# Kernel tuning notes

Hardware: AMD Instinct MI355X
Metric: run time of the kernel (lower is better)

Reference implementation:

```python
import jax, jax.numpy as jnp
import numpy as np

B, T, D, H = 4, 2048, 1024, 32  # batch, positions, embed_dim, max_history (buffer full)
DECAY_RATE = 0.95


def setup_inputs() -> dict:
    key = jax.random.key(0)
    ks = jax.random.split(key, 10)
    s = 1.0 / np.sqrt(D)
    return {
        "x": jax.random.normal(ks[0], (B, T, D), dtype=jnp.float32),
        "history": jax.random.normal(ks[1], (T, H, D), dtype=jnp.float32),
        "Wq": jax.random.normal(ks[2], (D, D), dtype=jnp.float32) * s,
        "bq": jax.random.normal(ks[3], (D,), dtype=jnp.float32) * 0.01,
        "Wk": jax.random.normal(ks[4], (D, D), dtype=jnp.float32) * s,
        "bk": jax.random.normal(ks[5], (D,), dtype=jnp.float32) * 0.01,
        "Wv": jax.random.normal(ks[6], (D, D), dtype=jnp.float32) * s,
        "bv": jax.random.normal(ks[7], (D,), dtype=jnp.float32) * 0.01,
        "Wo": jax.random.normal(ks[8], (D, D), dtype=jnp.float32) * s,
        "bo": jax.random.normal(ks[9], (D,), dtype=jnp.float32) * 0.01,
        "decay": jnp.power(jnp.float32(DECAY_RATE), jnp.arange(H, dtype=jnp.float32)),
    }


def reference(x, history, Wq, bq, Wk, bk, Wv, bv, Wo, bo, decay):
    # x: [B,T,D]; history: [T,H,D] (each position's own time history)
    d = x.shape[-1]
    Q = x @ Wq.T + bq                    # [B,T,D]
    K = history @ Wk.T + bk              # [T,H,D]
    V = history @ Wv.T + bv              # [T,H,D]
    # per-position attention over own history slice
    scores = jnp.einsum('btd,thd->bth', Q, K) / jnp.sqrt(jnp.float32(d))  # [B,T,H]
    bias = jnp.log(decay[::-1] + 1e-10)  # flipped log-decay, [H]
    attn = jax.nn.softmax(scores + bias, axis=-1)
    attended = jnp.einsum('bth,thd->btd', attn, V)  # [B,T,D]
    return (attended + x) @ Wo.T + bo
```

## Files before the change

kernel.cpp:

```cpp
#include <hip/hip_runtime.h>
#include <stdint.h>

#define B_ 4
#define T_ 2048
#define D_ 1024
#define H_ 32

typedef unsigned short u16;
typedef __attribute__((ext_vector_type(8))) short bf16x8;
typedef __attribute__((ext_vector_type(4))) float f32x4;

__device__ __forceinline__ u16 f2bf(float f) {
  union { float f; unsigned u; } c; c.f = f;
  unsigned r = 0x7fffu + ((c.u >> 16) & 1u);
  return (u16)((c.u + r) >> 16);
}
__device__ __forceinline__ float bf2f(u16 h) {
  union { unsigned u; float f; } c; c.u = ((unsigned)h) << 16;
  return c.f;
}

__device__ __forceinline__ void gload_lds16(const void* g, void* l) {
  __builtin_amdgcn_global_load_lds(
      (const __attribute__((address_space(1))) void*)g,
      (__attribute__((address_space(3))) void*)l, 16, 0, 0);
}

__global__ void megaprep(const float* __restrict__ x,
                         const float* __restrict__ Wq, const float* __restrict__ Wk,
                         const float* __restrict__ Wv, const float* __restrict__ Wo,
                         const float* __restrict__ bq, const float* __restrict__ bv,
                         const float* __restrict__ bo,
                         u16* __restrict__ xb,
                         u16* __restrict__ wqtb, u16* __restrict__ wktb,
                         u16* __restrict__ wvtb, u16* __restrict__ wob,
                         u16* __restrict__ b2w,
                         float* __restrict__ b2part, float* __restrict__ bvo) {
  const int bid = blockIdx.x;
  const int tid = threadIdx.x;
  if (bid < 4096) {
    const int z = bid >> 10, tile = bid & 1023;
    const int tx = tid & 31, ty = tid >> 5;
    const int c0 = (tile & 31) * 32, r0 = (tile >> 5) * 32;
    if (z == 3) {
#pragma unroll
      for (int r = 0; r < 32; r += 8) {
        const int row = r0 + ty + r, col = c0 + tx;
        const u16 v = f2bf(Wo[(size_t)row * D_ + col]);
        wob[(size_t)row * D_ + col] = v;
        b2w[(size_t)(D_ + row) * D_ + col] = v;
      }
      return;
    }
    const float* in = (z == 0) ? Wq : (z == 1) ? Wk : Wv;
    u16* out = (z == 0) ? wqtb : (z == 1) ? wktb : wvtb;
    __shared__ float tile_s[32][33];
#pragma unroll
    for (int r = 0; r < 32; r += 8)
      tile_s[ty + r][tx] = in[(size_t)(r0 + ty + r) * D_ + c0 + tx];
    __syncthreads();
#pragma unroll
    for (int r = 0; r < 32; r += 8)
      out[(size_t)(c0 + ty + r) * D_ + r0 + tx] = f2bf(tile_s[tx][ty + r]);
  } else if (bid < 6144) {
    const int base = (bid - 4096) * 1024;
#pragma unroll
    for (int k = 0; k < 4; ++k) {
      const int i4 = base + k * 256 + tid;
      float4 v = reinterpret_cast<const float4*>(x)[i4];
      ushort4 o;
      o.x = f2bf(v.x); o.y = f2bf(v.y); o.z = f2bf(v.z); o.w = f2bf(v.w);
      *reinterpret_cast<ushort4*>(xb + (size_t)i4 * 4) = o;
    }
  } else if (bid < 6208) {
    const int sub = bid - 6144;
    const int col = (sub & 3) * 256 + tid;
    const int j0 = (sub >> 2) * 64;
    float acc = 0.f;
#pragma unroll 8
    for (int j = 0; j < 64; ++j) acc += bq[j0 + j] * Wk[(size_t)(j0 + j) * D_ + col];
    b2part[(sub >> 2) * D_ + col] = acc;
  } else {
    const int wid = tid >> 6, lane = tid & 63;
    const int j = (bid - 6208) * 4 + wid;
    float acc = 0.f;
#pragma unroll
    for (int k4 = lane; k4 < 256; k4 += 64) {
      float4 w = *reinterpret_cast<const float4*>(Wo + (size_t)j * D_ + k4 * 4);
      float4 b = *reinterpret_cast<const float4*>(bv + k4 * 4);
      acc += w.x * b.x + w.y * b.y + w.z * b.z + w.w * b.w;
    }
#pragma unroll
    for (int m = 1; m < 64; m <<= 1) acc += __shfl_xor(acc, m);
    if (lane == 0) bvo[j] = acc + bo[j];
  }
}

__global__ void finish_kernel(const float* __restrict__ pk, const float* __restrict__ b2part,
                              const float* __restrict__ decay,
                              u16* __restrict__ b2w, u16* __restrict__ wvo,
                              float* __restrict__ bias2, float* __restrict__ logb) {
  const int bid = blockIdx.x;
  const int tid = threadIdx.x;
  if (bid < 2048) {
    const int tgt = bid >> 10;
    const int i4 = (bid & 1023) * 256 + tid;
    const int row = i4 >> 8, c4 = i4 & 255;
    const size_t slab = (size_t)D_ * D_;
    const size_t base = (size_t)tgt * 4 * slab + (size_t)row * D_ + c4 * 4;
    float4 a = *reinterpret_cast<const float4*>(pk + base);
    float4 b = *reinterpret_cast<const float4*>(pk + slab + base);
    float4 c = *reinterpret_cast<const float4*>(pk + 2 * slab + base);
    float4 d = *reinterpret_cast<const float4*>(pk + 3 * slab + base);
    ushort4 o;
    o.x = f2bf(a.x + b.x + c.x + d.x);
    o.y = f2bf(a.y + b.y + c.y + d.y);
    o.z = f2bf(a.z + b.z + c.z + d.z);
    o.w = f2bf(a.w + b.w + c.w + d.w);
    u16* out = tgt ? wvo : b2w;
    *reinterpret_cast<ushort4*>(out + (size_t)row * D_ + c4 * 4) = o;
  } else {
    const int col = (bid - 2048) * 256 + tid;
    float acc = 0.f;
#pragma unroll
    for (int jb = 0; jb < 16; ++jb) acc += b2part[jb * D_ + col];
    bias2[col] = acc;
    bias2[D_ + col] = 0.f;
    if (bid == 2048 && tid < H_)
      logb[tid] = __logf(decay[H_ - 1 - tid] + 1e-10f);
  }
}

template<int OUT_BF16, int ADDX>
__device__ __forceinline__ void gemm_core(
    const u16* __restrict__ A, const u16* __restrict__ Bw,
    const float* __restrict__ bias, const u16* __restrict__ xadd, int ldx,
    void* __restrict__ Cv, int K, int lda, int ldb, int ldc, int bm, int bn) {
  __shared__ u16 lA[128 * 32];
  __shared__ u16 lB[128 * 32];
  const int tid = threadIdx.x;
  const int w = tid >> 6, lane = tid & 63;
  const int wr = w >> 1, wc = w & 1;
  const int lr = lane & 15;
  const int lk = (lane >> 4) << 3;

  f32x4 acc[4][4] = {};

  const int c0 = tid, c1 = tid + 256;
  const size_t aoff0 = (size_t)(bm * 128 + (c0 >> 2)) * lda + ((c0 & 3) << 3);
  const size_t aoff1 = (size_t)(bm * 128 + (c1 >> 2)) * lda + ((c1 & 3) << 3);
  const size_t boff0 = (size_t)(bn * 128 + (c0 >> 2)) * ldb + ((c0 & 3) << 3);
  const size_t boff1 = (size_t)(bn * 128 + (c1 >> 2)) * ldb + ((c1 & 3) << 3);
  u16* lA0 = lA + c0 * 8; u16* lA1 = lA + c1 * 8;
  u16* lB0 = lB + c0 * 8; u16* lB1 = lB + c1 * 8;

  for (int k0 = 0; k0 < K; k0 += 32) {
    gload_lds16(A + aoff0 + k0, lA0);
    gload_lds16(A + aoff1 + k0, lA1);
    gload_lds16(Bw + boff0 + k0, lB0);
    gload_lds16(Bw + boff1 + k0, lB1);
    __syncthreads();
    bf16x8 aF[4], bF[4];
#pragma unroll
    for (int m = 0; m < 4; ++m)
      aF[m] = *reinterpret_cast<const bf16x8*>(&lA[(wr * 64 + m * 16 + lr) * 32 + lk]);
#pragma unroll
    for (int n = 0; n < 4; ++n)
      bF[n] = *reinterpret_cast<const bf16x8*>(&lB[(wc * 64 + n * 16 + lr) * 32 + lk]);
#pragma unroll
    for (int m = 0; m < 4; ++m)
#pragma unroll
      for (int n = 0; n < 4; ++n)
        acc[m][n] = __builtin_amdgcn_mfma_f32_16x16x32_bf16(aF[m], bF[n], acc[m][n], 0, 0, 0);
    __syncthreads();
  }

#pragma unroll
  for (int m = 0; m < 4; ++m) {
    const int row = bm * 128 + wr * 64 + m * 16 + ((lane >> 4) << 2);
#pragma unroll
    for (int n = 0; n < 4; ++n) {
      const int col = bn * 128 + wc * 64 + n * 16 + lr;
      const float bb = bias ? bias[col] : 0.f;
#pragma unroll
      for (int r = 0; r < 4; ++r) {
        float v = acc[m][n][r] + bb;
        if (ADDX) v += bf2f(xadd[(size_t)(row + r) * ldx + col]);
        if (OUT_BF16) ((u16*)Cv)[(size_t)(row + r) * ldc + col] = f2bf(v);
        else          ((float*)Cv)[(size_t)(row + r) * ldc + col] = v;
      }
    }
  }
}

template<int OUT_BF16, int ADDX>
__global__ __launch_bounds__(256, 2)
void gemm_bt(const u16* __restrict__ A, const u16* __restrict__ Bw,
             const float* __restrict__ bias, const u16* __restrict__ xadd, int ldx,
             void* __restrict__ Cv, int K, int lda, int ldb, int ldc) {
  gemm_core<OUT_BF16, ADDX>(A, Bw, bias, xadd, ldx, Cv, K, lda, ldb, ldc,
                            blockIdx.x, blockIdx.y);
}

__global__ __launch_bounds__(256, 2)
void gemm_splitk_dual(const u16* __restrict__ wktb, const u16* __restrict__ wqtb,
                      const u16* __restrict__ wob, const u16* __restrict__ wvtb,
                      float* __restrict__ pk) {
  const int z = blockIdx.z;
  const u16 *A, *B;
  if (z < 4) { A = wktb + z * 256; B = wqtb + z * 256; }
  else       { A = wob + (z - 4) * 256; B = wvtb + (z - 4) * 256; }
  float* C = pk + (size_t)z * D_ * D_;
  gemm_core<0, 0>(A, B, nullptr, nullptr, 0, C, 256, D_, D_, D_,
                  blockIdx.x, blockIdx.y);
}

__global__ __launch_bounds__(256, 2)
void attn_kernel(const u16* __restrict__ Q2, const float* __restrict__ hist,
                 const float* __restrict__ logb, u16* __restrict__ hw) {
  __shared__ u16 lh[H_ * D_];
  __shared__ float sTab[4][H_];
  __shared__ float pTab[H_][4];
  const int t = blockIdx.x;
  const int tid = threadIdx.x;
  const int w = tid >> 6, lane = tid & 63;
  const float* hp = hist + (size_t)t * (H_ * D_);

  float s[32] = {};
#pragma unroll 2
  for (int c = 0; c < 4; ++c) {
    const int d0 = lane * 4 + 256 * c;
    float qf[4][4];
#pragma unroll
    for (int b = 0; b < 4; ++b) {
      ushort4 qv = *reinterpret_cast<const ushort4*>(Q2 + ((size_t)b * T_ + t) * 2048 + d0);
      qf[b][0] = bf2f(qv.x); qf[b][1] = bf2f(qv.y);
      qf[b][2] = bf2f(qv.z); qf[b][3] = bf2f(qv.w);
    }
#pragma unroll
    for (int i = 0; i < 8; ++i) {
      const int h = w * 8 + i;
      float4 hv = *reinterpret_cast<const float4*>(hp + h * D_ + d0);
      ushort4 hb;
      hb.x = f2bf(hv.x); hb.y = f2bf(hv.y); hb.z = f2bf(hv.z); hb.w = f2bf(hv.w);
      *reinterpret_cast<ushort4*>(&lh[h * D_ + d0]) = hb;
#pragma unroll
      for (int b = 0; b < 4; ++b)
        s[b * 8 + i] += qf[b][0] * hv.x + qf[b][1] * hv.y +
                        qf[b][2] * hv.z + qf[b][3] * hv.w;
    }
  }
#pragma unroll
  for (int m = 1; m < 64; m <<= 1)
#pragma unroll
    for (int j = 0; j < 32; ++j) s[j] += __shfl_xor(s[j], m);
  if (lane < 32)
    sTab[lane >> 3][w * 8 + (lane & 7)] = s[lane] * 0.03125f + logb[w * 8 + (lane & 7)];
  __syncthreads();

  if (tid < 128) {
    const int b = tid >> 5, h = tid & 31;
    float m0 = -1e30f;
#pragma unroll
    for (int j = 0; j < 32; ++j) m0 = fmaxf(m0, sTab[b][j]);
    float sm = 0.f;
#pragma unroll
    for (int j = 0; j < 32; ++j) sm += __expf(sTab[b][j] - m0);
    pTab[h][b] = __expf(sTab[b][h] - m0) / sm;
  }
  __syncthreads();

  float acc[4][4] = {};
#pragma unroll 8
  for (int h = 0; h < H_; ++h) {
    ushort4 hv = *reinterpret_cast<const ushort4*>(&lh[h * D_ + tid * 4]);
    const float h0 = bf2f(hv.x), h1 = bf2f(hv.y), h2 = bf2f(hv.z), h3 = bf2f(hv.w);
    f32x4 pv = *reinterpret_cast<const f32x4*>(&pTab[h][0]);
#pragma unroll
    for (int bb = 0; bb < 4; ++bb) {
      acc[bb][0] += pv[bb] * h0;
      acc[bb][1] += pv[bb] * h1;
      acc[bb][2] += pv[bb] * h2;
      acc[bb][3] += pv[bb] * h3;
    }
  }
#pragma unroll
  for (int bb = 0; bb < 4; ++bb) {
    ushort4 o;
    o.x = f2bf(acc[bb][0]); o.y = f2bf(acc[bb][1]);
    o.z = f2bf(acc[bb][2]); o.w = f2bf(acc[bb][3]);
    *reinterpret_cast<ushort4*>(hw + ((size_t)bb * T_ + t) * D_ + tid * 4) = o;
  }
}

extern "C" void kernel_launch(void* const* d_in, const int* in_sizes, int n_in,
                              void* d_out, int out_size, void* d_ws, size_t ws_size,
                              hipStream_t stream) {
  (void)in_sizes; (void)n_in; (void)out_size; (void)ws_size;
  const float* x     = (const float*)d_in[0];
  const float* hist  = (const float*)d_in[1];
  const float* Wq    = (const float*)d_in[2];
  const float* bq    = (const float*)d_in[3];
  const float* Wk    = (const float*)d_in[4];
  const float* Wv    = (const float*)d_in[6];
  const float* bv    = (const float*)d_in[7];
  const float* Wo    = (const float*)d_in[8];
  const float* bo    = (const float*)d_in[9];
  const float* decay = (const float*)d_in[10];

  char* p = (char*)d_ws;
  u16* wqtb = (u16*)p; p += (size_t)D_ * D_ * 2;
  u16* wktb = (u16*)p; p += (size_t)D_ * D_ * 2;
  u16* wvtb = (u16*)p; p += (size_t)D_ * D_ * 2;
  u16* wob  = (u16*)p; p += (size_t)D_ * D_ * 2;
  u16* wvo  = (u16*)p; p += (size_t)D_ * D_ * 2;
  u16* b2w  = (u16*)p; p += (size_t)2 * D_ * D_ * 2;
  float* bias2  = (float*)p; p += 2 * D_ * 4;
  float* logb   = (float*)p; p += 4096;
  float* bvo    = (float*)p; p += 4096;
  float* b2part = (float*)p; p += 16 * D_ * 4;
  float* pk     = (float*)p; p += (size_t)8 * D_ * D_ * 4;
  u16* xb   = (u16*)p; p += (size_t)B_ * T_ * D_ * 2;
  u16* Q2b  = (u16*)p; p += (size_t)B_ * T_ * 2048 * 2;
  u16* hwb  = (u16*)p; p += (size_t)B_ * T_ * D_ * 2;

  const int M = B_ * T_;

  megaprep<<<6464, 256, 0, stream>>>(x, Wq, Wk, Wv, Wo, bq, bv, bo,
                                     xb, wqtb, wktb, wvtb, wob, b2w, b2part, bvo);
  gemm_splitk_dual<<<dim3(8, 8, 8), 256, 0, stream>>>(wktb, wqtb, wob, wvtb, pk);
  finish_kernel<<<2052, 256, 0, stream>>>(pk, b2part, decay, b2w, wvo, bias2, logb);

  gemm_bt<1, 0><<<dim3(M / 128, 2048 / 128), 256, 0, stream>>>(
      xb, b2w, bias2, nullptr, 0, Q2b, D_, D_, D_, 2048);
  attn_kernel<<<T_, 256, 0, stream>>>(Q2b, hist, logb, hwb);
  gemm_bt<0, 1><<<dim3(M / 128, D_ / 128), 256, 0, stream>>>(
      hwb, wvo, bvo, Q2b + 1024, 2048, (float*)d_out, D_, D_, D_, D_);
}
```

Baseline: 186.2 us.

## Replace 128x128 GEMMs with 256x256 triple-buffered swizzled-LDS GEMM kernel

Adds a new 512-thread GEMM kernel with 256x256 output tiles, a three-stage global-to-LDS pipeline using direct LDS loads, an XOR-swizzled LDS layout and a block-index remap that groups tiles. It replaces the two large activation GEMMs (the Q/K-fold projection and the output projection). It also halves the split-K factor of the weight-precombination GEMM, from 4 to 2 splits with K=512 each, which shrinks the partial buffer and the reduction in finish_kernel. The larger tiles are meant to raise data reuse and MFMA utilisation. The trade-off is fewer blocks (256 and 128) on a device with many CUs, plus higher register and LDS pressure per block.

```diff
diff --git a/kernel.cpp b/kernel.cpp
--- a/kernel.cpp
+++ b/kernel.cpp
@@ -107,16 +107,14 @@
     const int i4 = (bid & 1023) * 256 + tid;
     const int row = i4 >> 8, c4 = i4 & 255;
     const size_t slab = (size_t)D_ * D_;
-    const size_t base = (size_t)tgt * 4 * slab + (size_t)row * D_ + c4 * 4;
+    const size_t base = (size_t)tgt * 2 * slab + (size_t)row * D_ + c4 * 4;
     float4 a = *reinterpret_cast<const float4*>(pk + base);
     float4 b = *reinterpret_cast<const float4*>(pk + slab + base);
-    float4 c = *reinterpret_cast<const float4*>(pk + 2 * slab + base);
-    float4 d = *reinterpret_cast<const float4*>(pk + 3 * slab + base);
     ushort4 o;
-    o.x = f2bf(a.x + b.x + c.x + d.x);
-    o.y = f2bf(a.y + b.y + c.y + d.y);
-    o.z = f2bf(a.z + b.z + c.z + d.z);
-    o.w = f2bf(a.w + b.w + c.w + d.w);
+    o.x = f2bf(a.x + b.x);
+    o.y = f2bf(a.y + b.y);
+    o.z = f2bf(a.z + b.z);
+    o.w = f2bf(a.w + b.w);
     u16* out = tgt ? wvo : b2w;
     *reinterpret_cast<ushort4*>(out + (size_t)row * D_ + c4 * 4) = o;
   } else {
@@ -131,11 +129,9 @@
   }
 }
 
-template<int OUT_BF16, int ADDX>
 __device__ __forceinline__ void gemm_core(
     const u16* __restrict__ A, const u16* __restrict__ Bw,
-    const float* __restrict__ bias, const u16* __restrict__ xadd, int ldx,
-    void* __restrict__ Cv, int K, int lda, int ldb, int ldc, int bm, int bn) {
+    float* __restrict__ Cv, int K, int lda, int ldb, int ldc, int bm, int bn) {
   __shared__ u16 lA[128 * 32];
   __shared__ u16 lB[128 * 32];
   const int tid = threadIdx.x;
@@ -181,6 +177,103 @@
 #pragma unroll
     for (int n = 0; n < 4; ++n) {
       const int col = bn * 128 + wc * 64 + n * 16 + lr;
+#pragma unroll
+      for (int r = 0; r < 4; ++r)
+        Cv[(size_t)(row + r) * ldc + col] = acc[m][n][r];
+    }
+  }
+}
+
+__global__ __launch_bounds__(256, 2)
+void gemm_splitk_dual(const u16* __restrict__ wktb, const u16* __restrict__ wqtb,
+                      const u16* __restrict__ wob, const u16* __restrict__ wvtb,
+                      float* __restrict__ pk) {
+  const int z = blockIdx.z;
+  const u16 *A, *B;
+  if (z < 2) { A = wktb + z * 512; B = wqtb + z * 512; }
+  else       { A = wob + (z - 2) * 512; B = wvtb + (z - 2) * 512; }
+  float* C = pk + (size_t)z * D_ * D_;
+  gemm_core(A, B, C, 512, D_, D_, D_, blockIdx.x, blockIdx.y);
+}
+
+template<int OUT_BF16, int ADDX>
+__global__ __launch_bounds__(512, 2)
+void gemm256(const u16* __restrict__ A, const u16* __restrict__ Bw,
+             const float* __restrict__ bias, const u16* __restrict__ xadd, int ldx,
+             void* __restrict__ Cv, int K, int lda, int ldb, int ldc, int nbn) {
+  int bid = blockIdx.x;
+  { const int q = gridDim.x >> 3; bid = (bid & 7) * q + (bid >> 3); }
+  const int bm = bid / nbn, bn = bid % nbn;
+
+  __shared__ __attribute__((aligned(16))) u16 lds[3 * 16384];
+  const int tid = threadIdx.x;
+  const int wid = tid >> 6, lane = tid & 63;
+  const int wm = wid >> 2, wn = wid & 3;
+  const int lr = lane & 15, ls = lane >> 4;
+
+  f32x4 acc[8][4] = {};
+
+  const int r0s = tid >> 2, sl = tid & 3;
+
+  const int NT = K >> 5;
+#define STAGE(kt, buf)                                                          \
+  {                                                                             \
+    const int k0_ = (kt) << 5;                                                  \
+    u16* la_ = lds + (buf) * 16384;                                             \
+    u16* lb_ = la_ + 8192;                                                      \
+    _Pragma("unroll")                                                           \
+    for (int L = 0; L < 2; ++L) {                                               \
+      const int r_ = L * 128 + r0s;                                             \
+      const int cs_ = sl ^ ((r_ >> 1) & 3);                                     \
+      gload_lds16(A + (size_t)(bm * 256 + r_) * lda + k0_ + cs_ * 8,            \
+                  la_ + (size_t)L * 4096 + (size_t)tid * 8);                    \
+      gload_lds16(Bw + (size_t)(bn * 256 + r_) * ldb + k0_ + cs_ * 8,           \
+                  lb_ + (size_t)L * 4096 + (size_t)tid * 8);                    \
+    }                                                                           \
+  }
+
+  STAGE(0, 0);
+  STAGE(1, 1);
+  asm volatile("s_waitcnt vmcnt(4)" ::: "memory");
+  __builtin_amdgcn_sched_barrier(0);
+  __builtin_amdgcn_s_barrier();
+
+  for (int t = 0; t < NT; ++t) {
+    const int buf = t % 3;
+    if (t + 2 < NT) STAGE(t + 2, (t + 2) % 3);
+    const char* la = (const char*)(lds + buf * 16384);
+    const char* lb = la + 16384;
+    bf16x8 aF[8], bF[4];
+#pragma unroll
+    for (int n = 0; n < 4; ++n) {
+      const int row = wn * 64 + n * 16 + lr;
+      bF[n] = *reinterpret_cast<const bf16x8*>(lb + row * 64 + ((ls ^ ((row >> 1) & 3)) << 4));
+    }
+#pragma unroll
+    for (int m = 0; m < 8; ++m) {
+      const int row = wm * 128 + m * 16 + lr;
+      aF[m] = *reinterpret_cast<const bf16x8*>(la + row * 64 + ((ls ^ ((row >> 1) & 3)) << 4));
+    }
+    __builtin_amdgcn_s_setprio(1);
+#pragma unroll
+    for (int m = 0; m < 8; ++m)
+#pragma unroll
+      for (int n = 0; n < 4; ++n)
+        acc[m][n] = __builtin_amdgcn_mfma_f32_16x16x32_bf16(aF[m], bF[n], acc[m][n], 0, 0, 0);
+    __builtin_amdgcn_s_setprio(0);
+    if (t + 2 < NT) asm volatile("s_waitcnt vmcnt(4)" ::: "memory");
+    else            asm volatile("s_waitcnt vmcnt(0)" ::: "memory");
+    __builtin_amdgcn_sched_barrier(0);
+    __builtin_amdgcn_s_barrier();
+  }
+#undef STAGE
+
+#pragma unroll
+  for (int m = 0; m < 8; ++m) {
+    const int row = bm * 256 + wm * 128 + m * 16 + ls * 4;
+#pragma unroll
+    for (int n = 0; n < 4; ++n) {
+      const int col = bn * 256 + wn * 64 + n * 16 + lr;
       const float bb = bias ? bias[col] : 0.f;
 #pragma unroll
       for (int r = 0; r < 4; ++r) {
@@ -191,28 +284,6 @@
       }
     }
   }
-}
-
-template<int OUT_BF16, int ADDX>
-__global__ __launch_bounds__(256, 2)
-void gemm_bt(const u16* __restrict__ A, const u16* __restrict__ Bw,
-             const float* __restrict__ bias, const u16* __restrict__ xadd, int ldx,
-             void* __restrict__ Cv, int K, int lda, int ldb, int ldc) {
-  gemm_core<OUT_BF16, ADDX>(A, Bw, bias, xadd, ldx, Cv, K, lda, ldb, ldc,
-                            blockIdx.x, blockIdx.y);
-}
-
-__global__ __launch_bounds__(256, 2)
-void gemm_splitk_dual(const u16* __restrict__ wktb, const u16* __restrict__ wqtb,
-                      const u16* __restrict__ wob, const u16* __restrict__ wvtb,
-                      float* __restrict__ pk) {
-  const int z = blockIdx.z;
-  const u16 *A, *B;
-  if (z < 4) { A = wktb + z * 256; B = wqtb + z * 256; }
-  else       { A = wob + (z - 4) * 256; B = wvtb + (z - 4) * 256; }
-  float* C = pk + (size_t)z * D_ * D_;
-  gemm_core<0, 0>(A, B, nullptr, nullptr, 0, C, 256, D_, D_, D_,
-                  blockIdx.x, blockIdx.y);
 }
 
 __global__ __launch_bounds__(256, 2)
@@ -319,7 +390,7 @@
   float* logb   = (float*)p; p += 4096;
   float* bvo    = (float*)p; p += 4096;
   float* b2part = (float*)p; p += 16 * D_ * 4;
-  float* pk     = (float*)p; p += (size_t)8 * D_ * D_ * 4;
+  float* pk     = (float*)p; p += (size_t)4 * D_ * D_ * 4;
   u16* xb   = (u16*)p; p += (size_t)B_ * T_ * D_ * 2;
   u16* Q2b  = (u16*)p; p += (size_t)B_ * T_ * 2048 * 2;
   u16* hwb  = (u16*)p; p += (size_t)B_ * T_ * D_ * 2;
@@ -328,12 +399,12 @@
 
   megaprep<<<6464, 256, 0, stream>>>(x, Wq, Wk, Wv, Wo, bq, bv, bo,
                                      xb, wqtb, wktb, wvtb, wob, b2w, b2part, bvo);
-  gemm_splitk_dual<<<dim3(8, 8, 8), 256, 0, stream>>>(wktb, wqtb, wob, wvtb, pk);
+  gemm_splitk_dual<<<dim3(8, 8, 4), 256, 0, stream>>>(wktb, wqtb, wob, wvtb, pk);
   finish_kernel<<<2052, 256, 0, stream>>>(pk, b2part, decay, b2w, wvo, bias2, logb);
 
-  gemm_bt<1, 0><<<dim3(M / 128, 2048 / 128), 256, 0, stream>>>(
-      xb, b2w, bias2, nullptr, 0, Q2b, D_, D_, D_, 2048);
+  gemm256<1, 0><<<256, 512, 0, stream>>>(
+      xb, b2w, bias2, nullptr, 0, Q2b, D_, D_, D_, 2048, 8);
   attn_kernel<<<T_, 256, 0, stream>>>(Q2b, hist, logb, hwb);
-  gemm_bt<0, 1><<<dim3(M / 128, D_ / 128), 256, 0, stream>>>(
-      hwb, wvo, bvo, Q2b + 1024, 2048, (float*)d_out, D_, D_, D_, D_);
-}
+  gemm256<0, 1><<<128, 512, 0, stream>>>(
+      hwb, wvo, bvo, Q2b + 1024, 2048, (float*)d_out, D_, D_, D_, D_, 4);
+}
```

Result: slower. 195.2 us (+4.8%).
